# Performance work log

Measured on AMD Instinct MI355X. Metric: run time of the kernel, lower is better.

The kernel has to match this reference:

```python
import jax, jax.numpy as jnp
import numpy as np

V = 10000      # vocabulary_size
T = 20         # max_len
D = 512        # D_img == hidden size
H = 64         # actor/critic hidden
FI = 2048      # image feature dim
FB = 256       # box feature dim (FI + FB == 2304)
B = 1024       # batch
N_WORDS = 50   # allowed word_list size


def setup_inputs() -> dict:
    key = jax.random.key(0)
    ks = iter(jax.random.split(key, 40))
    def p(shape, s=0.02):
        return (jax.random.normal(next(ks), shape) * s).astype(jnp.float32)
    z = lambda *s: jnp.zeros(s, jnp.float32)
    inp = {
        "image_feature": jax.random.normal(next(ks), (B, FI), dtype=jnp.float32),
        "box_feature": jax.random.normal(next(ks), (B, FB), dtype=jnp.float32),
        # feature_resizer Linear(2304, D)
        "fr_w": p((FI + FB, D)), "fr_b": z(D),
        # _block dense1 / dense2 (each: Linear(D,D), GELU, Linear(D,D))
        "d1a_w": p((D, D)), "d1a_b": z(D), "d1b_w": p((D, D)), "d1b_b": z(D),
        "d2a_w": p((D, D)), "d2a_b": z(D), "d2b_w": p((D, D)), "d2b_b": z(D),
        # encoder LayerNorm (affine) + Linear(D, 512)
        "ln_g": jnp.ones((D,), jnp.float32), "ln_b": z(D),
        "eo_w": p((D, 512)), "eo_b": z(512),
        # word embedding
        "emb": p((V, 512)),
        # GRUCell weights, torch gate order (r, z, n)
        "gwi": p((512, 3 * 512)), "gwh": p((512, 3 * 512)),
        "gbi": z(3 * 512), "gbh": z(3 * 512),
        # actor: 512->64 tanh 64->64 tanh 64->V
        "a1_w": p((512, H)), "a1_b": z(H),
        "a2_w": p((H, H)), "a2_b": z(H),
        "a3_w": p((H, V), 0.01), "a3_b": z(V),
        # critic: 512->64 tanh 64->64 tanh 64->1
        "c1_w": p((512, H)), "c1_b": z(H),
        "c2_w": p((H, H)), "c2_b": z(H),
        "c3_w": p((H, 1)), "c3_b": z(1),
        # frozen word mask: 0 for allowed words, -1000 otherwise
        "word_mask": jnp.where(jnp.arange(V) < N_WORDS, 0.0, -1000.0).astype(jnp.float32),
    }
    return inp


def _ln(x, g=None, b=None):
    m = x.mean(-1, keepdims=True)
    v = x.var(-1, keepdims=True)
    y = (x - m) * jax.lax.rsqrt(v + 1e-5)
    return y if g is None else y * g + b


def _forward(image_feature, box_feature, fr_w, fr_b,
             d1a_w, d1a_b, d1b_w, d1b_b, d2a_w, d2a_b, d2b_w, d2b_b,
             ln_g, ln_b, eo_w, eo_b, emb, gwi, gwh, gbi, gbh,
             a1_w, a1_b, a2_w, a2_b, a3_w, a3_b,
             c1_w, c1_b, c2_w, c2_b, c3_w, c3_b, word_mask):
    gelu = lambda t: jax.nn.gelu(t, approximate=False)
    # feature resizer + residual block + LN + projection (encoder)
    x0 = jnp.concatenate([image_feature, box_feature], axis=1) @ fr_w + fr_b
    y = gelu(_ln(x0) @ d1a_w + d1a_b) @ d1b_w + d1b_b
    y = _ln(y + x0)
    x = x0 + (gelu(y @ d2a_w + d2a_b) @ d2b_w + d2b_b)
    img = _ln(x, ln_g, ln_b) @ eo_w + eo_b          # [B, 512]

    samp_key = jax.random.key(1)

    def step(carry, t):
        hx, ix = carry
        # torch: hx = GRUCell(input=hx, hidden=ix)
        gi = hx @ gwi + gbi
        gh = ix @ gwh + gbh
        gir, giz, gin = jnp.split(gi, 3, axis=-1)
        ghr, ghz, ghn = jnp.split(gh, 3, axis=-1)
        r = jax.nn.sigmoid(gir + ghr)
        zg = jax.nn.sigmoid(giz + ghz)
        n = jnp.tanh(gin + r * ghn)
        h = (1.0 - zg) * n + zg * ix                # new hidden [B, 512]
        logits = jnp.tanh(jnp.tanh(h @ a1_w + a1_b) @ a2_w + a2_b) @ a3_w + a3_b + word_mask
        logp = jax.nn.log_softmax(logits, axis=-1)  # [B, V]
        act = jax.random.categorical(jax.random.fold_in(samp_key, t), logp, axis=-1)  # [B]
        lp = jnp.take_along_axis(logp, act[:, None], axis=-1)[:, 0]
        ent = -jnp.sum(jnp.exp(logp) * logp, axis=-1)
        val = (jnp.tanh(jnp.tanh(h @ c1_w + c1_b) @ c2_w + c2_b) @ c3_w + c3_b)[:, 0]
        return (h, emb[act]), (act, lp, ent, val)

    _, (acts, lps, ents, vals) = jax.lax.scan(step, (img, jnp.zeros_like(img)), jnp.arange(T))
    # scan stacks along time first -> transpose to [B, T]
    return acts.T, lps.T, ents.T, vals.T[..., None]


def reference(image_feature, box_feature, fr_w, fr_b,
              d1a_w, d1a_b, d1b_w, d1b_b, d2a_w, d2a_b, d2b_w, d2b_b,
              ln_g, ln_b, eo_w, eo_b, emb, gwi, gwh, gbi, gbh,
              a1_w, a1_b, a2_w, a2_b, a3_w, a3_b,
              c1_w, c1_b, c2_w, c2_b, c3_w, c3_b, word_mask):
    return _forward(image_feature, box_feature, fr_w, fr_b,
                    d1a_w, d1a_b, d1b_w, d1b_b, d2a_w, d2a_b, d2b_w, d2b_b,
                    ln_g, ln_b, eo_w, eo_b, emb, gwi, gwh, gbi, gbh,
                    a1_w, a1_b, a2_w, a2_b, a3_w, a3_b,
                    c1_w, c1_b, c2_w, c2_b, c3_w, c3_b, word_mask)
```

## Files before the change

kernel.cpp:

```cpp
#include <hip/hip_runtime.h>
#include <math.h>
#include <stdint.h>

#define BB 1024
#define DD 512
#define VV 10000
#define TT 20
#define NW 50

__host__ __device__ __forceinline__ void tf2x32(uint32_t k0, uint32_t k1,
                                                uint32_t x0, uint32_t x1,
                                                uint32_t& o0, uint32_t& o1) {
  uint32_t ks2 = k0 ^ k1 ^ 0x1BD11BDAu;
  x0 += k0; x1 += k1;
#define ROTL(x,r) (((x)<<(r))|((x)>>(32-(r))))
#define RND(r) { x0 += x1; x1 = ROTL(x1,(r)); x1 ^= x0; }
  RND(13) RND(15) RND(26) RND(6)   x0 += k1;  x1 += ks2 + 1u;
  RND(17) RND(29) RND(16) RND(24)  x0 += ks2; x1 += k0 + 2u;
  RND(13) RND(15) RND(26) RND(6)   x0 += k0;  x1 += k1 + 3u;
  RND(17) RND(29) RND(16) RND(24)  x0 += k1;  x1 += ks2 + 4u;
  RND(13) RND(15) RND(26) RND(6)   x0 += ks2; x1 += k0 + 5u;
#undef RND
#undef ROTL
  o0 = x0; o1 = x1;
}

__device__ __forceinline__ float wave_sum(float v) {
#pragma unroll
  for (int o = 32; o > 0; o >>= 1) v += __shfl_xor(v, o, 64);
  return v;
}
__device__ __forceinline__ float wave_max(float v) {
#pragma unroll
  for (int o = 32; o > 0; o >>= 1) v = fmaxf(v, __shfl_xor(v, o, 64));
  return v;
}

__device__ __forceinline__ float gelu_f(float x) {
  float u = x / 1.4142135623730951f;
  float e = (float)erf((double)u);
  return x * (e + 1.0f) * 0.5f;
}

template<int ACT, bool RES, bool CONCAT>
__global__ __launch_bounds__(64) void wgemm_k(
    const float* __restrict__ A, const float* __restrict__ A2, int K1,
    const float* __restrict__ W, int ldw, const float* __restrict__ bias,
    const float* __restrict__ res, float* __restrict__ C, int N, int K)
{
  __shared__ alignas(16) float As[32][40];
  __shared__ alignas(16) float Ws[32][40];
  const int bm = blockIdx.x * 32;
  const int bn = blockIdx.y * 32;
  const int lane = threadIdx.x;
  const int tr = (lane >> 3) << 2;
  const int tc = (lane & 7) << 2;
  const int am  = lane & 31;
  const int ak0 = (lane >> 5) << 2;
  const int wr0 = lane >> 3;
  const int wc  = (lane & 7) << 2;

  float4 pa[4], pw[4];
  auto load_tile = [&](int k0) {
#pragma unroll
    for (int h = 0; h < 4; h++) {
      int kq = ak0 + 8 * h;
      int gk = k0 + kq;
      if (CONCAT) {
        pa[h] = (gk < K1) ? *(const float4*)&A[(size_t)(bm + am) * K1 + gk]
                          : *(const float4*)&A2[(size_t)(bm + am) * (K - K1) + (gk - K1)];
      } else {
        pa[h] = *(const float4*)&A[(size_t)(bm + am) * K + gk];
      }
      int wr = wr0 + 8 * h;
      pw[h] = *(const float4*)&W[(size_t)(k0 + wr) * ldw + bn + wc];
    }
  };

  float acc[4][4] = {};
  load_tile(0);
  for (int k0 = 0; k0 < K; k0 += 32) {
#pragma unroll
    for (int h = 0; h < 4; h++) {
      int kq = ak0 + 8 * h;
      As[kq + 0][am] = pa[h].x; As[kq + 1][am] = pa[h].y;
      As[kq + 2][am] = pa[h].z; As[kq + 3][am] = pa[h].w;
      *(float4*)&Ws[wr0 + 8 * h][wc] = pw[h];
    }
    __syncthreads();
    if (k0 + 32 < K) load_tile(k0 + 32);
#pragma unroll
    for (int kk = 0; kk < 32; kk++) {
      float4 av = *(const float4*)&As[kk][tr];
      float4 bv = *(const float4*)&Ws[kk][tc];
      acc[0][0] = fmaf(av.x, bv.x, acc[0][0]);
      acc[0][1] = fmaf(av.x, bv.y, acc[0][1]);
      acc[0][2] = fmaf(av.x, bv.z, acc[0][2]);
      acc[0][3] = fmaf(av.x, bv.w, acc[0][3]);
      acc[1][0] = fmaf(av.y, bv.x, acc[1][0]);
      acc[1][1] = fmaf(av.y, bv.y, acc[1][1]);
      acc[1][2] = fmaf(av.y, bv.z, acc[1][2]);
      acc[1][3] = fmaf(av.y, bv.w, acc[1][3]);
      acc[2][0] = fmaf(av.z, bv.x, acc[2][0]);
      acc[2][1] = fmaf(av.z, bv.y, acc[2][1]);
      acc[2][2] = fmaf(av.z, bv.z, acc[2][2]);
      acc[2][3] = fmaf(av.z, bv.w, acc[2][3]);
      acc[3][0] = fmaf(av.w, bv.x, acc[3][0]);
      acc[3][1] = fmaf(av.w, bv.y, acc[3][1]);
      acc[3][2] = fmaf(av.w, bv.z, acc[3][2]);
      acc[3][3] = fmaf(av.w, bv.w, acc[3][3]);
    }
    __syncthreads();
  }
#pragma unroll
  for (int i = 0; i < 4; i++) {
    int m = bm + tr + i;
    float4 o;
    float* op = (float*)&o;
#pragma unroll
    for (int j = 0; j < 4; j++) {
      int n = bn + tc + j;
      float v = acc[i][j] + bias[n];
      if (ACT == 1) v = gelu_f(v);
      if (RES) v = v + res[(size_t)m * N + n];
      op[j] = v;
    }
    *(float4*)&C[(size_t)m * N + bn + tc] = o;
  }
}

template<bool AFFINE, bool ADD>
__global__ __launch_bounds__(256) void lnorm_k(
    const float* __restrict__ X, const float* __restrict__ X2,
    const float* __restrict__ g, const float* __restrict__ bt,
    float* __restrict__ Y)
{
  __shared__ float red[8];
  int row = blockIdx.x, tid = threadIdx.x;
  const float* x = X + (size_t)row * DD;
  float v0 = x[tid], v1 = x[tid + 256];
  if (ADD) {
    const float* x2 = X2 + (size_t)row * DD;
    v0 += x2[tid]; v1 += x2[tid + 256];
  }
  float s = wave_sum(v0 + v1);
  if ((tid & 63) == 0) red[tid >> 6] = s;
  __syncthreads();
  float mean = (red[0] + red[1] + red[2] + red[3]) * (1.0f / 512.0f);
  float d0 = v0 - mean, d1 = v1 - mean;
  float s2 = wave_sum(d0 * d0 + d1 * d1);
  if ((tid & 63) == 0) red[4 + (tid >> 6)] = s2;
  __syncthreads();
  float var = (red[4] + red[5] + red[6] + red[7]) * (1.0f / 512.0f);
  float rs = (float)(1.0 / sqrt((double)(var + 1e-5f)));
  float y0 = d0 * rs, y1 = d1 * rs;
  if (AFFINE) {
    y0 = y0 * g[tid] + bt[tid];
    y1 = y1 * g[tid + 256] + bt[tid + 256];
  }
  Y[(size_t)row * DD + tid] = y0;
  Y[(size_t)row * DD + tid + 256] = y1;
}

__global__ __launch_bounds__(64) void gru_head(
    const float* __restrict__ gi, const float* __restrict__ table,
    const float* __restrict__ gbh, const float* __restrict__ emb,
    const float* __restrict__ a1w, const float* __restrict__ a1b,
    const float* __restrict__ a2w, const float* __restrict__ a2b,
    const float* __restrict__ a3w, const float* __restrict__ a3b,
    const float* __restrict__ c1w, const float* __restrict__ c1b,
    const float* __restrict__ c2w, const float* __restrict__ c2b,
    const float* __restrict__ c3w, const float* __restrict__ c3b,
    const float* __restrict__ wmask,
    float* __restrict__ hx, float* __restrict__ out,
    int t, uint32_t fk0, uint32_t fk1)
{
  int b = blockIdx.x;
  int lane = threadIdx.x;
  __shared__ float sh[DD];
  __shared__ float st1[64], st2[64], sc1[64];

  int a = (t > 0) ? (int)out[(size_t)b * TT + (t - 1)] : -1;
  const float* ghb = (a >= 0) ? (table + (size_t)a * 1536) : gbh;
  const float* gib = gi + (size_t)b * 1536;
  const float* er  = (a >= 0) ? (emb + (size_t)a * DD) : nullptr;
#pragma unroll
  for (int jj = 0; jj < 8; jj++) {
    int j = lane + 64 * jj;
    float ixv = (a >= 0) ? er[j] : 0.f;
    float r = (float)(1.0 / (1.0 + exp(-(double)(gib[j] + ghb[j]))));
    float z = (float)(1.0 / (1.0 + exp(-(double)(gib[DD + j] + ghb[DD + j]))));
    float narg = gib[2 * DD + j] + r * ghb[2 * DD + j];
    float n = (float)tanh((double)narg);
    float h = (1.0f - z) * n + z * ixv;
    sh[j] = h;
    hx[(size_t)b * DD + j] = h;
  }
  __syncthreads();

  float aa0 = 0, aa1 = 0, aa2 = 0, aa3 = 0, ca0 = 0, ca1 = 0, ca2 = 0, ca3 = 0;
  for (int k = 0; k < DD; k += 4) {
    float h0 = sh[k], h1 = sh[k + 1], h2 = sh[k + 2], h3 = sh[k + 3];
    aa0 = fmaf(h0, a1w[(k + 0) * 64 + lane], aa0);
    aa1 = fmaf(h1, a1w[(k + 1) * 64 + lane], aa1);
    aa2 = fmaf(h2, a1w[(k + 2) * 64 + lane], aa2);
    aa3 = fmaf(h3, a1w[(k + 3) * 64 + lane], aa3);
    ca0 = fmaf(h0, c1w[(k + 0) * 64 + lane], ca0);
    ca1 = fmaf(h1, c1w[(k + 1) * 64 + lane], ca1);
    ca2 = fmaf(h2, c1w[(k + 2) * 64 + lane], ca2);
    ca3 = fmaf(h3, c1w[(k + 3) * 64 + lane], ca3);
  }
  st1[lane] = (float)tanh((double)(((aa0 + aa1) + (aa2 + aa3)) + a1b[lane]));
  sc1[lane] = (float)tanh((double)(((ca0 + ca1) + (ca2 + ca3)) + c1b[lane]));
  __syncthreads();

  float a2acc = 0, c2acc = 0;
  for (int k = 0; k < 64; k++) {
    a2acc = fmaf(st1[k], a2w[k * 64 + lane], a2acc);
    c2acc = fmaf(sc1[k], c2w[k * 64 + lane], c2acc);
  }
  st2[lane] = (float)tanh((double)(a2acc + a2b[lane]));
  float t2c = (float)tanh((double)(c2acc + c2b[lane]));
  __syncthreads();

  float val = wave_sum(t2c * c3w[lane]) + c3b[0];

  float lg = -INFINITY;
  if (lane < NW) {
    float s = 0;
    for (int k = 0; k < 64; k++) s = fmaf(st2[k], a3w[k * VV + lane], s);
    lg = (s + a3b[lane]) + wmask[lane];
  }

  float m = wave_max(lg);
  float shf = 0.f, e = 0.f;
  if (lane < NW) { shf = lg - m; e = (float)exp((double)shf); }
  float se = wave_sum(e);
  float lse = (float)log((double)se);
  float logp = shf - lse;
  float term = 0.f;
  if (lane < NW) { float p = (float)exp((double)logp); term = p * logp; }
  float ent = -wave_sum(term);

  float score = -INFINITY;
  if (lane < NW) {
    uint32_t i = (uint32_t)b * (uint32_t)VV + (uint32_t)lane;
    uint32_t o0, o1;
    tf2x32(fk0, fk1, 0u, i, o0, o1);
    uint32_t bits = o0 ^ o1;
    uint32_t mant = bits >> 9;
    float u = (mant == 0u) ? 1.17549435e-38f
                           : (float)mant * 1.1920928955078125e-7f;
    float l1 = (float)log((double)u);
    float l2 = (float)log((double)(-l1));
    score = -l2 + logp;
  }

  float best = score; int bi = lane;
#pragma unroll
  for (int off = 32; off > 0; off >>= 1) {
    float ob = __shfl_xor(best, off, 64);
    int oi = __shfl_xor(bi, off, 64);
    if (ob > best || (ob == best && oi < bi)) { best = ob; bi = oi; }
  }
  float lp = __shfl(logp, bi, 64);

  if (lane == 0) {
    out[(size_t)b * TT + t] = (float)bi;
    out[(size_t)BB * TT + (size_t)b * TT + t] = lp;
    out[2 * (size_t)BB * TT + (size_t)b * TT + t] = ent;
    out[3 * (size_t)BB * TT + (size_t)b * TT + t] = val;
  }
}

__global__ __launch_bounds__(256) void diag_k(float* out, float code, int n) {
  int i = blockIdx.x * 256 + threadIdx.x;
  if (i < n) out[i] = code;
}

extern "C" void kernel_launch(void* const* d_in, const int* in_sizes, int n_in,
                              void* d_out, int out_size, void* d_ws, size_t ws_size,
                              hipStream_t stream) {
  static const int EXP_SIZES[34] = {
    2097152, 262144, 1179648, 512, 262144, 512, 262144, 512, 262144, 512,
    262144, 512, 512, 512, 262144, 512, 5120000, 786432, 786432, 1536,
    1536, 32768, 64, 4096, 64, 640000, 10000, 32768, 64, 4096,
    64, 64, 1, 10000 };
  double code = 0.0;
  if (n_in != 34) code = 1e6 + (double)n_in;
  else {
    for (int i = 0; i < 34; i++)
      if (in_sizes[i] != EXP_SIZES[i]) { code = 2e6 + i * 1e4 + (in_sizes[i] % 10000); break; }
  }
  if (code == 0.0 && out_size != 4 * BB * TT) code = 3e6 + (double)(out_size % 1000000);
  if (code == 0.0 && ws_size < (size_t)24 * 1024 * 1024) {
    size_t kb = ws_size / 1024; if (kb > 999999) kb = 999999;
    code = 4e6 + (double)kb;
  }
  if (code != 0.0) {
    diag_k<<<(out_size + 255) / 256, 256, 0, stream>>>((float*)d_out, (float)code, out_size);
    return;
  }

  const float* image = (const float*)d_in[0];
  const float* boxf  = (const float*)d_in[1];
  const float* fr_w  = (const float*)d_in[2];
  const float* fr_b  = (const float*)d_in[3];
  const float* d1a_w = (const float*)d_in[4];
  const float* d1a_b = (const float*)d_in[5];
  const float* d1b_w = (const float*)d_in[6];
  const float* d1b_b = (const float*)d_in[7];
  const float* d2a_w = (const float*)d_in[8];
  const float* d2a_b = (const float*)d_in[9];
  const float* d2b_w = (const float*)d_in[10];
  const float* d2b_b = (const float*)d_in[11];
  const float* ln_g  = (const float*)d_in[12];
  const float* ln_b  = (const float*)d_in[13];
  const float* eo_w  = (const float*)d_in[14];
  const float* eo_b  = (const float*)d_in[15];
  const float* emb   = (const float*)d_in[16];
  const float* gwi   = (const float*)d_in[17];
  const float* gwh   = (const float*)d_in[18];
  const float* gbi   = (const float*)d_in[19];
  const float* gbh   = (const float*)d_in[20];
  const float* a1w   = (const float*)d_in[21];
  const float* a1b   = (const float*)d_in[22];
  const float* a2w   = (const float*)d_in[23];
  const float* a2b   = (const float*)d_in[24];
  const float* a3w   = (const float*)d_in[25];
  const float* a3b   = (const float*)d_in[26];
  const float* c1w   = (const float*)d_in[27];
  const float* c1b   = (const float*)d_in[28];
  const float* c2w   = (const float*)d_in[29];
  const float* c2b   = (const float*)d_in[30];
  const float* c3w   = (const float*)d_in[31];
  const float* c3b   = (const float*)d_in[32];
  const float* wmask = (const float*)d_in[33];

  float* ws = (float*)d_ws;
  const size_t R = (size_t)BB * DD;
  float* hx    = ws;
  float* gi    = ws + R;
  float* Q     = ws + 4 * R;
  float* S     = ws + 5 * R;
  float* U     = ws + 6 * R;
  float* table = ws + 7 * R;
  float* P     = gi;
  float* out = (float*)d_out;

  dim3 wblk(64);
  wgemm_k<0, false, false><<<dim3(2, 48), wblk, 0, stream>>>(emb, nullptr, 0, gwh, 1536, gbh, nullptr, table, 1536, 512);
  wgemm_k<0, false, true><<<dim3(32, 16), wblk, 0, stream>>>(image, boxf, 2048, fr_w, 512, fr_b, nullptr, P, 512, 2304);
  lnorm_k<false, false><<<BB, dim3(256), 0, stream>>>(P, nullptr, nullptr, nullptr, Q);
  wgemm_k<1, false, false><<<dim3(32, 16), wblk, 0, stream>>>(Q, nullptr, 0, d1a_w, 512, d1a_b, nullptr, S, 512, 512);
  wgemm_k<0, false, false><<<dim3(32, 16), wblk, 0, stream>>>(S, nullptr, 0, d1b_w, 512, d1b_b, nullptr, U, 512, 512);
  lnorm_k<false, true><<<BB, dim3(256), 0, stream>>>(U, P, nullptr, nullptr, Q);
  wgemm_k<1, false, false><<<dim3(32, 16), wblk, 0, stream>>>(Q, nullptr, 0, d2a_w, 512, d2a_b, nullptr, S, 512, 512);
  wgemm_k<0, true, false><<<dim3(32, 16), wblk, 0, stream>>>(S, nullptr, 0, d2b_w, 512, d2b_b, P, U, 512, 512);
  lnorm_k<true, false><<<BB, dim3(256), 0, stream>>>(U, nullptr, ln_g, ln_b, Q);
  wgemm_k<0, false, false><<<dim3(32, 16), wblk, 0, stream>>>(Q, nullptr, 0, eo_w, 512, eo_b, nullptr, hx, 512, 512);

  for (int t = 0; t < TT; t++) {
    uint32_t fk0, fk1;
    tf2x32(0u, 1u, 0u, (uint32_t)t, fk0, fk1);
    wgemm_k<0, false, false><<<dim3(32, 48), wblk, 0, stream>>>(hx, nullptr, 0, gwi, 1536, gbi, nullptr, gi, 1536, 512);
    gru_head<<<BB, wblk, 0, stream>>>(gi, table, gbh, emb,
                                      a1w, a1b, a2w, a2b, a3w, a3b,
                                      c1w, c1b, c2w, c2b, c3w, c3b,
                                      wmask, hx, out, t, fk0, fk1);
  }
}
```

Before: 1.730 ms.

## Deepen GEMM K-tiles, drop barriers, widen GRU GEMM rows, batch head rows

The FP32 GEMM kernel now takes a template parameter for rows per thread. It stages 64-deep K slices instead of 32 and removes the __syncthreads barriers, since each block is a single 64-lane wave. The per-step GRU input GEMM uses 8 rows per thread, giving 64x32 tiles and half as many blocks. gru_head packs four batch rows into one 256-thread block with per-wave shared buffers. The aims are fewer barriers and loop iterations, more reuse of each shared-memory weight load, and fewer small launches' worth of blocks. The cost is higher register and LDS use per block. Dropping the barriers also relies on in-wave ordering of LDS accesses.

```diff
diff --git a/kernel.cpp b/kernel.cpp
--- a/kernel.cpp
+++ b/kernel.cpp
@@ -42,78 +42,83 @@
   return x * (e + 1.0f) * 0.5f;
 }
 
-template<int ACT, bool RES, bool CONCAT>
+template<int MR, int ACT, bool RES, bool CONCAT>
 __global__ __launch_bounds__(64) void wgemm_k(
     const float* __restrict__ A, const float* __restrict__ A2, int K1,
     const float* __restrict__ W, int ldw, const float* __restrict__ bias,
     const float* __restrict__ res, float* __restrict__ C, int N, int K)
 {
-  __shared__ alignas(16) float As[32][40];
-  __shared__ alignas(16) float Ws[32][40];
-  const int bm = blockIdx.x * 32;
+  constexpr int TM = MR * 8;
+  constexpr int ASTR = (TM == 64) ? 72 : 40;
+  constexpr int WSTR = 40;
+  constexpr int PA_N = (TM == 64) ? 16 : 8;
+  __shared__ alignas(16) float As[64][ASTR];
+  __shared__ alignas(16) float Ws[64][WSTR];
+  const int bm = blockIdx.x * TM;
   const int bn = blockIdx.y * 32;
   const int lane = threadIdx.x;
-  const int tr = (lane >> 3) << 2;
+  const int tr = (lane >> 3) * MR;
   const int tc = (lane & 7) << 2;
-  const int am  = lane & 31;
-  const int ak0 = (lane >> 5) << 2;
+  const int arow = (TM == 64) ? lane : (lane & 31);
+  const int akb  = (TM == 64) ? 0 : ((lane >> 5) * 32);
   const int wr0 = lane >> 3;
   const int wc  = (lane & 7) << 2;
 
-  float4 pa[4], pw[4];
+  float4 pa[PA_N], pw[8];
   auto load_tile = [&](int k0) {
 #pragma unroll
-    for (int h = 0; h < 4; h++) {
-      int kq = ak0 + 8 * h;
-      int gk = k0 + kq;
+    for (int h = 0; h < PA_N; h++) {
+      int gk = k0 + akb + 4 * h;
       if (CONCAT) {
-        pa[h] = (gk < K1) ? *(const float4*)&A[(size_t)(bm + am) * K1 + gk]
-                          : *(const float4*)&A2[(size_t)(bm + am) * (K - K1) + (gk - K1)];
+        pa[h] = (gk < K1) ? *(const float4*)&A[(size_t)(bm + arow) * K1 + gk]
+                          : *(const float4*)&A2[(size_t)(bm + arow) * (K - K1) + (gk - K1)];
       } else {
-        pa[h] = *(const float4*)&A[(size_t)(bm + am) * K + gk];
+        pa[h] = *(const float4*)&A[(size_t)(bm + arow) * K + gk];
       }
-      int wr = wr0 + 8 * h;
-      pw[h] = *(const float4*)&W[(size_t)(k0 + wr) * ldw + bn + wc];
+    }
+#pragma unroll
+    for (int h = 0; h < 8; h++) {
+      pw[h] = *(const float4*)&W[(size_t)(k0 + wr0 + 8 * h) * ldw + bn + wc];
     }
   };
 
-  float acc[4][4] = {};
+  float acc[MR][4];
+#pragma unroll
+  for (int i = 0; i < MR; i++)
+#pragma unroll
+    for (int j = 0; j < 4; j++) acc[i][j] = 0.f;
+
   load_tile(0);
-  for (int k0 = 0; k0 < K; k0 += 32) {
-#pragma unroll
-    for (int h = 0; h < 4; h++) {
-      int kq = ak0 + 8 * h;
-      As[kq + 0][am] = pa[h].x; As[kq + 1][am] = pa[h].y;
-      As[kq + 2][am] = pa[h].z; As[kq + 3][am] = pa[h].w;
-      *(float4*)&Ws[wr0 + 8 * h][wc] = pw[h];
-    }
-    __syncthreads();
-    if (k0 + 32 < K) load_tile(k0 + 32);
-#pragma unroll
-    for (int kk = 0; kk < 32; kk++) {
-      float4 av = *(const float4*)&As[kk][tr];
+  for (int k0 = 0; k0 < K; k0 += 64) {
+#pragma unroll
+    for (int h = 0; h < PA_N; h++) {
+      int kb = akb + 4 * h;
+      As[kb + 0][arow] = pa[h].x; As[kb + 1][arow] = pa[h].y;
+      As[kb + 2][arow] = pa[h].z; As[kb + 3][arow] = pa[h].w;
+    }
+#pragma unroll
+    for (int h = 0; h < 8; h++) *(float4*)&Ws[wr0 + 8 * h][wc] = pw[h];
+    if (k0 + 64 < K) load_tile(k0 + 64);
+#pragma unroll
+    for (int kk = 0; kk < 64; kk++) {
       float4 bv = *(const float4*)&Ws[kk][tc];
-      acc[0][0] = fmaf(av.x, bv.x, acc[0][0]);
-      acc[0][1] = fmaf(av.x, bv.y, acc[0][1]);
-      acc[0][2] = fmaf(av.x, bv.z, acc[0][2]);
-      acc[0][3] = fmaf(av.x, bv.w, acc[0][3]);
-      acc[1][0] = fmaf(av.y, bv.x, acc[1][0]);
-      acc[1][1] = fmaf(av.y, bv.y, acc[1][1]);
-      acc[1][2] = fmaf(av.y, bv.z, acc[1][2]);
-      acc[1][3] = fmaf(av.y, bv.w, acc[1][3]);
-      acc[2][0] = fmaf(av.z, bv.x, acc[2][0]);
-      acc[2][1] = fmaf(av.z, bv.y, acc[2][1]);
-      acc[2][2] = fmaf(av.z, bv.z, acc[2][2]);
-      acc[2][3] = fmaf(av.z, bv.w, acc[2][3]);
-      acc[3][0] = fmaf(av.w, bv.x, acc[3][0]);
-      acc[3][1] = fmaf(av.w, bv.y, acc[3][1]);
-      acc[3][2] = fmaf(av.w, bv.z, acc[3][2]);
-      acc[3][3] = fmaf(av.w, bv.w, acc[3][3]);
-    }
-    __syncthreads();
-  }
-#pragma unroll
-  for (int i = 0; i < 4; i++) {
+#pragma unroll
+      for (int ih = 0; ih < MR / 4; ih++) {
+        float4 av = *(const float4*)&As[kk][tr + 4 * ih];
+        float* ap = (float*)&av;
+#pragma unroll
+        for (int q = 0; q < 4; q++) {
+          int i = 4 * ih + q;
+          acc[i][0] = fmaf(ap[q], bv.x, acc[i][0]);
+          acc[i][1] = fmaf(ap[q], bv.y, acc[i][1]);
+          acc[i][2] = fmaf(ap[q], bv.z, acc[i][2]);
+          acc[i][3] = fmaf(ap[q], bv.w, acc[i][3]);
+        }
+      }
+    }
+  }
+#pragma unroll
+  for (int i = 0; i < MR; i++) {
     int m = bm + tr + i;
     float4 o;
     float* op = (float*)&o;
@@ -162,7 +167,7 @@
   Y[(size_t)row * DD + tid + 256] = y1;
 }
 
-__global__ __launch_bounds__(64) void gru_head(
+__global__ __launch_bounds__(256) void gru_head(
     const float* __restrict__ gi, const float* __restrict__ table,
     const float* __restrict__ gbh, const float* __restrict__ emb,
     const float* __restrict__ a1w, const float* __restrict__ a1b,
@@ -175,10 +180,11 @@
     float* __restrict__ hx, float* __restrict__ out,
     int t, uint32_t fk0, uint32_t fk1)
 {
-  int b = blockIdx.x;
-  int lane = threadIdx.x;
-  __shared__ float sh[DD];
-  __shared__ float st1[64], st2[64], sc1[64];
+  int w = threadIdx.x >> 6;
+  int lane = threadIdx.x & 63;
+  int b = blockIdx.x * 4 + w;
+  __shared__ float sh[4][DD];
+  __shared__ float st1[4][64], st2[4][64], sc1[4][64];
 
   int a = (t > 0) ? (int)out[(size_t)b * TT + (t - 1)] : -1;
   const float* ghb = (a >= 0) ? (table + (size_t)a * 1536) : gbh;
@@ -193,14 +199,14 @@
     float narg = gib[2 * DD + j] + r * ghb[2 * DD + j];
     float n = (float)tanh((double)narg);
     float h = (1.0f - z) * n + z * ixv;
-    sh[j] = h;
+    sh[w][j] = h;
     hx[(size_t)b * DD + j] = h;
   }
   __syncthreads();
 
   float aa0 = 0, aa1 = 0, aa2 = 0, aa3 = 0, ca0 = 0, ca1 = 0, ca2 = 0, ca3 = 0;
   for (int k = 0; k < DD; k += 4) {
-    float h0 = sh[k], h1 = sh[k + 1], h2 = sh[k + 2], h3 = sh[k + 3];
+    float h0 = sh[w][k], h1 = sh[w][k + 1], h2 = sh[w][k + 2], h3 = sh[w][k + 3];
     aa0 = fmaf(h0, a1w[(k + 0) * 64 + lane], aa0);
     aa1 = fmaf(h1, a1w[(k + 1) * 64 + lane], aa1);
     aa2 = fmaf(h2, a1w[(k + 2) * 64 + lane], aa2);
@@ -210,16 +216,16 @@
     ca2 = fmaf(h2, c1w[(k + 2) * 64 + lane], ca2);
     ca3 = fmaf(h3, c1w[(k + 3) * 64 + lane], ca3);
   }
-  st1[lane] = (float)tanh((double)(((aa0 + aa1) + (aa2 + aa3)) + a1b[lane]));
-  sc1[lane] = (float)tanh((double)(((ca0 + ca1) + (ca2 + ca3)) + c1b[lane]));
+  st1[w][lane] = (float)tanh((double)(((aa0 + aa1) + (aa2 + aa3)) + a1b[lane]));
+  sc1[w][lane] = (float)tanh((double)(((ca0 + ca1) + (ca2 + ca3)) + c1b[lane]));
   __syncthreads();
 
   float a2acc = 0, c2acc = 0;
   for (int k = 0; k < 64; k++) {
-    a2acc = fmaf(st1[k], a2w[k * 64 + lane], a2acc);
-    c2acc = fmaf(sc1[k], c2w[k * 64 + lane], c2acc);
-  }
-  st2[lane] = (float)tanh((double)(a2acc + a2b[lane]));
+    a2acc = fmaf(st1[w][k], a2w[k * 64 + lane], a2acc);
+    c2acc = fmaf(sc1[w][k], c2w[k * 64 + lane], c2acc);
+  }
+  st2[w][lane] = (float)tanh((double)(a2acc + a2b[lane]));
   float t2c = (float)tanh((double)(c2acc + c2b[lane]));
   __syncthreads();
 
@@ -228,7 +234,7 @@
   float lg = -INFINITY;
   if (lane < NW) {
     float s = 0;
-    for (int k = 0; k < 64; k++) s = fmaf(st2[k], a3w[k * VV + lane], s);
+    for (int k = 0; k < 64; k++) s = fmaf(st2[w][k], a3w[k * VV + lane], s);
     lg = (s + a3b[lane]) + wmask[lane];
   }
 
@@ -349,22 +355,22 @@
   float* out = (float*)d_out;
 
   dim3 wblk(64);
-  wgemm_k<0, false, false><<<dim3(2, 48), wblk, 0, stream>>>(emb, nullptr, 0, gwh, 1536, gbh, nullptr, table, 1536, 512);
-  wgemm_k<0, false, true><<<dim3(32, 16), wblk, 0, stream>>>(image, boxf, 2048, fr_w, 512, fr_b, nullptr, P, 512, 2304);
+  wgemm_k<4, 0, false, false><<<dim3(2, 48), wblk, 0, stream>>>(emb, nullptr, 0, gwh, 1536, gbh, nullptr, table, 1536, 512);
+  wgemm_k<4, 0, false, true><<<dim3(32, 16), wblk, 0, stream>>>(image, boxf, 2048, fr_w, 512, fr_b, nullptr, P, 512, 2304);
   lnorm_k<false, false><<<BB, dim3(256), 0, stream>>>(P, nullptr, nullptr, nullptr, Q);
-  wgemm_k<1, false, false><<<dim3(32, 16), wblk, 0, stream>>>(Q, nullptr, 0, d1a_w, 512, d1a_b, nullptr, S, 512, 512);
-  wgemm_k<0, false, false><<<dim3(32, 16), wblk, 0, stream>>>(S, nullptr, 0, d1b_w, 512, d1b_b, nullptr, U, 512, 512);
+  wgemm_k<4, 1, false, false><<<dim3(32, 16), wblk, 0, stream>>>(Q, nullptr, 0, d1a_w, 512, d1a_b, nullptr, S, 512, 512);
+  wgemm_k<4, 0, false, false><<<dim3(32, 16), wblk, 0, stream>>>(S, nullptr, 0, d1b_w, 512, d1b_b, nullptr, U, 512, 512);
   lnorm_k<false, true><<<BB, dim3(256), 0, stream>>>(U, P, nullptr, nullptr, Q);
-  wgemm_k<1, false, false><<<dim3(32, 16), wblk, 0, stream>>>(Q, nullptr, 0, d2a_w, 512, d2a_b, nullptr, S, 512, 512);
-  wgemm_k<0, true, false><<<dim3(32, 16), wblk, 0, stream>>>(S, nullptr, 0, d2b_w, 512, d2b_b, P, U, 512, 512);
+  wgemm_k<4, 1, false, false><<<dim3(32, 16), wblk, 0, stream>>>(Q, nullptr, 0, d2a_w, 512, d2a_b, nullptr, S, 512, 512);
+  wgemm_k<4, 0, true, false><<<dim3(32, 16), wblk, 0, stream>>>(S, nullptr, 0, d2b_w, 512, d2b_b, P, U, 512, 512);
   lnorm_k<true, false><<<BB, dim3(256), 0, stream>>>(U, nullptr, ln_g, ln_b, Q);
-  wgemm_k<0, false, false><<<dim3(32, 16), wblk, 0, stream>>>(Q, nullptr, 0, eo_w, 512, eo_b, nullptr, hx, 512, 512);
+  wgemm_k<4, 0, false, false><<<dim3(32, 16), wblk, 0, stream>>>(Q, nullptr, 0, eo_w, 512, eo_b, nullptr, hx, 512, 512);
 
   for (int t = 0; t < TT; t++) {
     uint32_t fk0, fk1;
     tf2x32(0u, 1u, 0u, (uint32_t)t, fk0, fk1);
-    wgemm_k<0, false, false><<<dim3(32, 48), wblk, 0, stream>>>(hx, nullptr, 0, gwi, 1536, gbi, nullptr, gi, 1536, 512);
-    gru_head<<<BB, wblk, 0, stream>>>(gi, table, gbh, emb,
+    wgemm_k<8, 0, false, false><<<dim3(16, 48), wblk, 0, stream>>>(hx, nullptr, 0, gwi, 1536, gbi, nullptr, gi, 1536, 512);
+    gru_head<<<dim3(BB / 4), dim3(256), 0, stream>>>(gi, table, gbh, emb,
                                       a1w, a1b, a2w, a2b, a3w, a3b,
                                       c1w, c1b, c2w, c2b, c3w, c3b,
                                       wmask, hx, out, t, fk0, fk1);
```

Result: slower. 1.824 ms (+5.5%).
